# Optimization experiments

Measured on AMD Instinct MI355X. Metric: run time of the kernel, lower is better.

## Reference

```python
import jax, jax.numpy as jnp
import numpy as np

HIDDEN_DIM = 512


def setup_inputs() -> dict:
    key = jax.random.key(0)
    ks = jax.random.split(key, 7)
    B, SQ, SKV, DIN, H = 8, 2048, 2048, 1024, HIDDEN_DIM
    query = jax.random.normal(ks[0], (B, SQ, H), dtype=jnp.float32)
    states = jax.random.normal(ks[1], (B, SKV, DIN), dtype=jnp.float32)
    mask = jax.random.uniform(ks[2], (B, SQ, SKV), dtype=jnp.float32)
    # LazyLinear params (stored as [in, out]; torch uses x @ W.T with W [out, in])
    Wk = jax.random.normal(ks[3], (DIN, H), dtype=jnp.float32) * (1.0 / np.sqrt(DIN))
    bk = jax.random.normal(ks[4], (H,), dtype=jnp.float32) * 0.02
    Wv = jax.random.normal(ks[5], (DIN, H), dtype=jnp.float32) * (1.0 / np.sqrt(DIN))
    bv = jax.random.normal(ks[6], (H,), dtype=jnp.float32) * 0.02
    return {"query": query, "states": states, "mask": mask,
            "Wk": Wk, "bk": bk, "Wv": Wv, "bv": bv}


def reference(query, states, mask, Wk, bk, Wv, bv):
    # transform_states=True: project states into key/value spaces
    keys = states @ Wk + bk        # [B, S_kv, H]
    values = states @ Wv + bv      # [B, S_kv, H]
    # bmm(query, keys^T) / sqrt(H)
    scale = 1.0 / jnp.sqrt(jnp.asarray(keys.shape[-1], dtype=query.dtype))
    scores = jnp.einsum('bqh,bkh->bqk', query, keys) * scale  # [B, S_q, S_kv]
    scores = mask * scores  # multiplicative mask
    # source detaches the softmax output
    attn = jax.lax.stop_gradient(jax.nn.softmax(scores, axis=-1))
    return jnp.einsum('bqk,bkh->bqh', attn, values)  # [B, S_q, H]
```

## Files before the change

kernel.cpp:

```cpp
#include <hip/hip_runtime.h>
#include <hip/hip_bf16.h>
#include <stdint.h>

#define BM 128
#define BN 128
#define BK 32

typedef __bf16 bf16;
typedef bf16 bf16x8 __attribute__((ext_vector_type(8)));
typedef float f32x4 __attribute__((ext_vector_type(4)));

typedef const __attribute__((address_space(1))) void* gas1_t;
typedef __attribute__((address_space(3))) void* las3_t;

__device__ __forceinline__ void gl_lds16(const void* g, void* l) {
  __builtin_amdgcn_global_load_lds((gas1_t)g, (las3_t)l, 16, 0, 0);
}

__device__ __forceinline__ void gemm_core(const bf16* A, const bf16* Bt,
                                          int lda, int ldb, int kTiles,
                                          bf16* As, bf16* Bs, f32x4 acc[4][4]) {
  const int tid = threadIdx.x;
  const int lane = tid & 63;
  const int wid = tid >> 6;
  const int wr = wid >> 1, wc = wid & 1;
  const int lr = lane & 15, lg = lane >> 4;

  for (int kt = 0; kt < kTiles; ++kt) {
    const bf16* Ak = A + kt * BK;
    const bf16* Bk = Bt + kt * BK;
#pragma unroll
    for (int p = 0; p < 2; ++p) {
      int c = p * 256 + tid;
      int row = c >> 2, k8 = (c & 3) << 3;
      gl_lds16(Ak + (size_t)row * lda + k8, As + c * 8);
      gl_lds16(Bk + (size_t)row * ldb + k8, Bs + c * 8);
    }
    __syncthreads();
    bf16x8 af[4], bfr[4];
#pragma unroll
    for (int i = 0; i < 4; ++i) {
      af[i]  = *(const bf16x8*)(As + (wr * 64 + i * 16 + lr) * BK + lg * 8);
      bfr[i] = *(const bf16x8*)(Bs + (wc * 64 + i * 16 + lr) * BK + lg * 8);
    }
#pragma unroll
    for (int i = 0; i < 4; ++i)
#pragma unroll
      for (int j = 0; j < 4; ++j)
        acc[i][j] = __builtin_amdgcn_mfma_f32_16x16x32_bf16(af[i], bfr[j], acc[i][j], 0, 0, 0);
    __syncthreads();
  }
}

__global__ __launch_bounds__(256) void k_cast(const float* __restrict__ in,
                                              bf16* __restrict__ out, int n8) {
  int i = blockIdx.x * blockDim.x + threadIdx.x;
  int stride = gridDim.x * blockDim.x;
  for (; i < n8; i += stride) {
    float4 a = ((const float4*)in)[2 * (size_t)i];
    float4 b = ((const float4*)in)[2 * (size_t)i + 1];
    bf16x8 o;
    o[0] = (bf16)a.x; o[1] = (bf16)a.y; o[2] = (bf16)a.z; o[3] = (bf16)a.w;
    o[4] = (bf16)b.x; o[5] = (bf16)b.y; o[6] = (bf16)b.z; o[7] = (bf16)b.w;
    ((bf16x8*)out)[i] = o;
  }
}

__global__ __launch_bounds__(256) void k_buildwt(const float* __restrict__ Wk,
                                                 const float* __restrict__ Wv,
                                                 bf16* __restrict__ Wt) {
  int n = blockIdx.x;
  const float* W = (n < 512) ? Wk : Wv;
  int col = n & 511;
  for (int k = threadIdx.x; k < 1024; k += 256)
    Wt[(size_t)n * 1024 + k] = (bf16)W[(size_t)k * 512 + col];
}

__global__ __launch_bounds__(256) void k_proj(const bf16* __restrict__ S,
                                              const bf16* __restrict__ Wt,
                                              const float* __restrict__ bk,
                                              const float* __restrict__ bv,
                                              bf16* __restrict__ Kb,
                                              bf16* __restrict__ VT) {
  __shared__ bf16 As[BM * BK], Bs[BN * BK];
  f32x4 acc[4][4] = {};
  int m0 = blockIdx.x * BM, n0 = blockIdx.y * BN;
  gemm_core(S + (size_t)m0 * 1024, Wt + (size_t)n0 * 1024, 1024, 1024, 1024 / BK, As, Bs, acc);
  const int lane = threadIdx.x & 63, wid = threadIdx.x >> 6;
  const int wr = wid >> 1, wc = wid & 1, lr = lane & 15, lg = lane >> 4;
#pragma unroll
  for (int i = 0; i < 4; ++i) {
    int gmb = m0 + wr * 64 + i * 16 + lg * 4;
#pragma unroll
    for (int j = 0; j < 4; ++j) {
      int gn = n0 + wc * 64 + j * 16 + lr;
      f32x4 v = acc[i][j];
      if (gn < 512) {
        float bias = bk[gn];
#pragma unroll
        for (int r = 0; r < 4; ++r)
          Kb[(size_t)(gmb + r) * 512 + gn] = (bf16)(v[r] + bias);
      } else {
        float bias = bv[gn - 512];
#pragma unroll
        for (int r = 0; r < 4; ++r) {
          int gm = gmb + r, b = gm >> 11, s = gm & 2047;
          VT[((size_t)(b * 512 + (gn - 512))) * 2048 + s] = (bf16)(v[r] + bias);
        }
      }
    }
  }
}

__global__ __launch_bounds__(256) void k_scores(const bf16* __restrict__ Qb,
                                                const bf16* __restrict__ Kb,
                                                const float* __restrict__ mask,
                                                bf16* __restrict__ P,
                                                float* __restrict__ lsum) {
  __shared__ bf16 As[BM * BK], Bs[BN * BK];
  f32x4 acc[4][4] = {};
  int b = blockIdx.z;
  int m0 = blockIdx.x * BM, n0 = blockIdx.y * BN;
  gemm_core(Qb + (size_t)b * 2048 * 512 + (size_t)m0 * 512,
            Kb + (size_t)b * 2048 * 512 + (size_t)n0 * 512, 512, 512, 512 / BK, As, Bs, acc);
  const float scale = 0.04419417382415922f;
  const float* Mb = mask + (size_t)b * 2048 * 2048;
  bf16* Pb = P + (size_t)b * 2048 * 2048;
  const int lane = threadIdx.x & 63, wid = threadIdx.x >> 6;
  const int wr = wid >> 1, wc = wid & 1, lr = lane & 15, lg = lane >> 4;
  float rs[4][4];
#pragma unroll
  for (int i = 0; i < 4; ++i)
#pragma unroll
    for (int r = 0; r < 4; ++r) rs[i][r] = 0.f;
#pragma unroll
  for (int i = 0; i < 4; ++i) {
    int gmb = m0 + wr * 64 + i * 16 + lg * 4;
#pragma unroll
    for (int j = 0; j < 4; ++j) {
      int gn = n0 + wc * 64 + j * 16 + lr;
      f32x4 v = acc[i][j];
#pragma unroll
      for (int r = 0; r < 4; ++r) {
        size_t off = (size_t)(gmb + r) * 2048 + gn;
        float p = __expf(v[r] * scale * Mb[off]);
        Pb[off] = (bf16)p;
        rs[i][r] += p;
      }
    }
  }
#pragma unroll
  for (int i = 0; i < 4; ++i)
#pragma unroll
    for (int r = 0; r < 4; ++r) {
      float v = rs[i][r];
      v += __shfl_xor(v, 1, 16);
      v += __shfl_xor(v, 2, 16);
      v += __shfl_xor(v, 4, 16);
      v += __shfl_xor(v, 8, 16);
      if (lr == 0)
        atomicAdd(&lsum[b * 2048 + m0 + wr * 64 + i * 16 + lg * 4 + r], v);
    }
}

__global__ __launch_bounds__(256) void k_pv(const bf16* __restrict__ P,
                                            const bf16* __restrict__ VT,
                                            const float* __restrict__ lsum,
                                            float* __restrict__ out) {
  __shared__ bf16 As[BM * BK], Bs[BN * BK];
  f32x4 acc[4][4] = {};
  int b = blockIdx.z;
  int m0 = blockIdx.x * BM, n0 = blockIdx.y * BN;
  gemm_core(P + (size_t)b * 2048 * 2048 + (size_t)m0 * 2048,
            VT + (size_t)b * 512 * 2048 + (size_t)n0 * 2048, 2048, 2048, 2048 / BK, As, Bs, acc);
  float* Ob = out + (size_t)b * 2048 * 512;
  const float* lb = lsum + b * 2048;
  const int lane = threadIdx.x & 63, wid = threadIdx.x >> 6;
  const int wr = wid >> 1, wc = wid & 1, lr = lane & 15, lg = lane >> 4;
#pragma unroll
  for (int i = 0; i < 4; ++i) {
    int gmb = m0 + wr * 64 + i * 16 + lg * 4;
#pragma unroll
    for (int j = 0; j < 4; ++j) {
      int gn = n0 + wc * 64 + j * 16 + lr;
      f32x4 v = acc[i][j];
#pragma unroll
      for (int r = 0; r < 4; ++r)
        Ob[(size_t)(gmb + r) * 512 + gn] = v[r] / lb[gmb + r];
    }
  }
}

extern "C" void kernel_launch(void* const* d_in, const int* in_sizes, int n_in,
                              void* d_out, int out_size, void* d_ws, size_t ws_size,
                              hipStream_t stream) {
  const float* query  = (const float*)d_in[0];
  const float* states = (const float*)d_in[1];
  const float* mask   = (const float*)d_in[2];
  const float* Wk     = (const float*)d_in[3];
  const float* bk     = (const float*)d_in[4];
  const float* Wv     = (const float*)d_in[5];
  const float* bv     = (const float*)d_in[6];
  float* out = (float*)d_out;

  char* ws = (char*)d_ws;
  bf16* WT = (bf16*)(ws);
  bf16* Qb = (bf16*)(ws + (2ull << 20));
  bf16* Kb = (bf16*)(ws + (18ull << 20));
  bf16* VT = (bf16*)(ws + (34ull << 20));
  bf16* Sb = (bf16*)(ws + (50ull << 20));
  bf16* P  = (bf16*)(ws + (50ull << 20));
  float* ls = (float*)(ws + (114ull << 20));

  hipMemsetAsync(ls, 0, 8 * 2048 * sizeof(float), stream);
  k_buildwt<<<dim3(1024), 256, 0, stream>>>(Wk, Wv, WT);
  k_cast<<<dim3(2048), 256, 0, stream>>>(states, Sb, 16384 * 1024 / 8);
  k_cast<<<dim3(1024), 256, 0, stream>>>(query, Qb, 8 * 2048 * 512 / 8);
  k_proj<<<dim3(128, 8), 256, 0, stream>>>(Sb, WT, bk, bv, Kb, VT);
  k_scores<<<dim3(16, 16, 8), 256, 0, stream>>>(Qb, Kb, mask, P, ls);
  k_pv<<<dim3(16, 4, 8), 256, 0, stream>>>(P, VT, ls, out);
}
```

Before: 453.0 us.

## Swap GEMM operand roles so epilogues write contiguous vectors

Swaps the A/B operands of the score, PV and key-projection GEMMs so each lane's four accumulator rows land on contiguous memory. Mask reads, P writes, K writes and output writes become float4/bf16x4 vector accesses instead of strided scalar ones. The combined K/V projection is split into two kernels, each with a layout-friendly epilogue. The weight transpose now goes through an LDS tile for coalescing. Risks are more kernel launches and changed tile order and cache locality.

```diff
diff --git a/kernel.cpp b/kernel.cpp
--- a/kernel.cpp
+++ b/kernel.cpp
@@ -7,6 +7,7 @@
 #define BK 32
 
 typedef __bf16 bf16;
+typedef bf16 bf16x4 __attribute__((ext_vector_type(4)));
 typedef bf16 bf16x8 __attribute__((ext_vector_type(8)));
 typedef float f32x4 __attribute__((ext_vector_type(4)));
 
@@ -66,127 +67,145 @@
   }
 }
 
-__global__ __launch_bounds__(256) void k_buildwt(const float* __restrict__ Wk,
-                                                 const float* __restrict__ Wv,
-                                                 bf16* __restrict__ Wt) {
-  int n = blockIdx.x;
-  const float* W = (n < 512) ? Wk : Wv;
-  int col = n & 511;
-  for (int k = threadIdx.x; k < 1024; k += 256)
-    Wt[(size_t)n * 1024 + k] = (bf16)W[(size_t)k * 512 + col];
-}
-
-__global__ __launch_bounds__(256) void k_proj(const bf16* __restrict__ S,
-                                              const bf16* __restrict__ Wt,
-                                              const float* __restrict__ bk,
-                                              const float* __restrict__ bv,
-                                              bf16* __restrict__ Kb,
-                                              bf16* __restrict__ VT) {
-  __shared__ bf16 As[BM * BK], Bs[BN * BK];
-  f32x4 acc[4][4] = {};
-  int m0 = blockIdx.x * BM, n0 = blockIdx.y * BN;
-  gemm_core(S + (size_t)m0 * 1024, Wt + (size_t)n0 * 1024, 1024, 1024, 1024 / BK, As, Bs, acc);
+__global__ __launch_bounds__(256) void k_transposeW(const float* __restrict__ Wk,
+                                                    const float* __restrict__ Wv,
+                                                    bf16* __restrict__ WT) {
+  __shared__ float t[32][33];
+  const float* W = blockIdx.z ? Wv : Wk;
+  bf16* O = WT + (size_t)blockIdx.z * 512 * 1024;
+  int h0 = blockIdx.x * 32, d0 = blockIdx.y * 32;
+  int tx = threadIdx.x & 31, ty = threadIdx.x >> 5;
+#pragma unroll
+  for (int yy = 0; yy < 4; ++yy)
+    t[ty + yy * 8][tx] = W[(size_t)(d0 + ty + yy * 8) * 512 + h0 + tx];
+  __syncthreads();
+#pragma unroll
+  for (int yy = 0; yy < 4; ++yy)
+    O[(size_t)(h0 + ty + yy * 8) * 1024 + d0 + tx] = (bf16)t[tx][ty + yy * 8];
+}
+
+__global__ __launch_bounds__(256) void k_projK(const bf16* __restrict__ WkT,
+                                               const bf16* __restrict__ S,
+                                               const float* __restrict__ bk,
+                                               bf16* __restrict__ Kb) {
+  __shared__ bf16 As[BM * BK], Bs[BN * BK];
+  f32x4 acc[4][4] = {};
+  int h0 = blockIdx.x * BM, t0 = blockIdx.y * BN;
+  gemm_core(WkT + (size_t)h0 * 1024, S + (size_t)t0 * 1024, 1024, 1024, 1024 / BK, As, Bs, acc);
   const int lane = threadIdx.x & 63, wid = threadIdx.x >> 6;
   const int wr = wid >> 1, wc = wid & 1, lr = lane & 15, lg = lane >> 4;
 #pragma unroll
   for (int i = 0; i < 4; ++i) {
-    int gmb = m0 + wr * 64 + i * 16 + lg * 4;
+    int hb = h0 + wr * 64 + i * 16 + lg * 4;
+    float4 bias = *(const float4*)(bk + hb);
 #pragma unroll
     for (int j = 0; j < 4; ++j) {
-      int gn = n0 + wc * 64 + j * 16 + lr;
-      f32x4 v = acc[i][j];
-      if (gn < 512) {
-        float bias = bk[gn];
-#pragma unroll
-        for (int r = 0; r < 4; ++r)
-          Kb[(size_t)(gmb + r) * 512 + gn] = (bf16)(v[r] + bias);
-      } else {
-        float bias = bv[gn - 512];
-#pragma unroll
-        for (int r = 0; r < 4; ++r) {
-          int gm = gmb + r, b = gm >> 11, s = gm & 2047;
-          VT[((size_t)(b * 512 + (gn - 512))) * 2048 + s] = (bf16)(v[r] + bias);
-        }
-      }
-    }
-  }
-}
-
-__global__ __launch_bounds__(256) void k_scores(const bf16* __restrict__ Qb,
-                                                const bf16* __restrict__ Kb,
+      int t = t0 + wc * 64 + j * 16 + lr;
+      f32x4 v = acc[i][j];
+      bf16x4 o;
+      o[0] = (bf16)(v[0] + bias.x); o[1] = (bf16)(v[1] + bias.y);
+      o[2] = (bf16)(v[2] + bias.z); o[3] = (bf16)(v[3] + bias.w);
+      *(bf16x4*)(Kb + (size_t)t * 512 + hb) = o;
+    }
+  }
+}
+
+__global__ __launch_bounds__(256) void k_projV(const bf16* __restrict__ S,
+                                               const bf16* __restrict__ WvT,
+                                               const float* __restrict__ bv,
+                                               bf16* __restrict__ VT) {
+  __shared__ bf16 As[BM * BK], Bs[BN * BK];
+  f32x4 acc[4][4] = {};
+  int t0 = blockIdx.x * BM, h0 = blockIdx.y * BN;
+  gemm_core(S + (size_t)t0 * 1024, WvT + (size_t)h0 * 1024, 1024, 1024, 1024 / BK, As, Bs, acc);
+  const int lane = threadIdx.x & 63, wid = threadIdx.x >> 6;
+  const int wr = wid >> 1, wc = wid & 1, lr = lane & 15, lg = lane >> 4;
+#pragma unroll
+  for (int i = 0; i < 4; ++i) {
+    int tb = t0 + wr * 64 + i * 16 + lg * 4;
+    int b = tb >> 11, s = tb & 2047;
+#pragma unroll
+    for (int j = 0; j < 4; ++j) {
+      int h = h0 + wc * 64 + j * 16 + lr;
+      float bias = bv[h];
+      f32x4 v = acc[i][j];
+      bf16x4 o;
+      o[0] = (bf16)(v[0] + bias); o[1] = (bf16)(v[1] + bias);
+      o[2] = (bf16)(v[2] + bias); o[3] = (bf16)(v[3] + bias);
+      *(bf16x4*)(VT + ((size_t)(b * 512 + h)) * 2048 + s) = o;
+    }
+  }
+}
+
+__global__ __launch_bounds__(256) void k_scores(const bf16* __restrict__ Kb,
+                                                const bf16* __restrict__ Qb,
                                                 const float* __restrict__ mask,
                                                 bf16* __restrict__ P,
                                                 float* __restrict__ lsum) {
   __shared__ bf16 As[BM * BK], Bs[BN * BK];
   f32x4 acc[4][4] = {};
   int b = blockIdx.z;
-  int m0 = blockIdx.x * BM, n0 = blockIdx.y * BN;
-  gemm_core(Qb + (size_t)b * 2048 * 512 + (size_t)m0 * 512,
-            Kb + (size_t)b * 2048 * 512 + (size_t)n0 * 512, 512, 512, 512 / BK, As, Bs, acc);
+  int kv0 = blockIdx.x * BM, q0 = blockIdx.y * BN;
+  gemm_core(Kb + (size_t)b * 2048 * 512 + (size_t)kv0 * 512,
+            Qb + (size_t)b * 2048 * 512 + (size_t)q0 * 512, 512, 512, 512 / BK, As, Bs, acc);
   const float scale = 0.04419417382415922f;
   const float* Mb = mask + (size_t)b * 2048 * 2048;
   bf16* Pb = P + (size_t)b * 2048 * 2048;
   const int lane = threadIdx.x & 63, wid = threadIdx.x >> 6;
   const int wr = wid >> 1, wc = wid & 1, lr = lane & 15, lg = lane >> 4;
-  float rs[4][4];
-#pragma unroll
-  for (int i = 0; i < 4; ++i)
-#pragma unroll
-    for (int r = 0; r < 4; ++r) rs[i][r] = 0.f;
-#pragma unroll
-  for (int i = 0; i < 4; ++i) {
-    int gmb = m0 + wr * 64 + i * 16 + lg * 4;
-#pragma unroll
-    for (int j = 0; j < 4; ++j) {
-      int gn = n0 + wc * 64 + j * 16 + lr;
-      f32x4 v = acc[i][j];
-#pragma unroll
-      for (int r = 0; r < 4; ++r) {
-        size_t off = (size_t)(gmb + r) * 2048 + gn;
-        float p = __expf(v[r] * scale * Mb[off]);
-        Pb[off] = (bf16)p;
-        rs[i][r] += p;
-      }
-    }
-  }
-#pragma unroll
-  for (int i = 0; i < 4; ++i)
-#pragma unroll
-    for (int r = 0; r < 4; ++r) {
-      float v = rs[i][r];
-      v += __shfl_xor(v, 1, 16);
-      v += __shfl_xor(v, 2, 16);
-      v += __shfl_xor(v, 4, 16);
-      v += __shfl_xor(v, 8, 16);
-      if (lr == 0)
-        atomicAdd(&lsum[b * 2048 + m0 + wr * 64 + i * 16 + lg * 4 + r], v);
-    }
-}
-
-__global__ __launch_bounds__(256) void k_pv(const bf16* __restrict__ P,
-                                            const bf16* __restrict__ VT,
+  float rs[4] = {0.f, 0.f, 0.f, 0.f};
+#pragma unroll
+  for (int j = 0; j < 4; ++j) {
+    int q = q0 + wc * 64 + j * 16 + lr;
+    size_t qrow = (size_t)q * 2048;
+#pragma unroll
+    for (int i = 0; i < 4; ++i) {
+      int kvb = kv0 + wr * 64 + i * 16 + lg * 4;
+      float4 m4 = *(const float4*)(Mb + qrow + kvb);
+      f32x4 v = acc[i][j];
+      float p0 = __expf(v[0] * scale * m4.x);
+      float p1 = __expf(v[1] * scale * m4.y);
+      float p2 = __expf(v[2] * scale * m4.z);
+      float p3 = __expf(v[3] * scale * m4.w);
+      bf16x4 o; o[0] = (bf16)p0; o[1] = (bf16)p1; o[2] = (bf16)p2; o[3] = (bf16)p3;
+      *(bf16x4*)(Pb + qrow + kvb) = o;
+      rs[j] += p0 + p1 + p2 + p3;
+    }
+  }
+#pragma unroll
+  for (int j = 0; j < 4; ++j) {
+    float v = rs[j];
+    v += __shfl_xor(v, 16);
+    v += __shfl_xor(v, 32);
+    if (lane < 16)
+      atomicAdd(&lsum[b * 2048 + q0 + wc * 64 + j * 16 + lr], v);
+  }
+}
+
+__global__ __launch_bounds__(256) void k_pv(const bf16* __restrict__ VT,
+                                            const bf16* __restrict__ P,
                                             const float* __restrict__ lsum,
                                             float* __restrict__ out) {
   __shared__ bf16 As[BM * BK], Bs[BN * BK];
   f32x4 acc[4][4] = {};
   int b = blockIdx.z;
-  int m0 = blockIdx.x * BM, n0 = blockIdx.y * BN;
-  gemm_core(P + (size_t)b * 2048 * 2048 + (size_t)m0 * 2048,
-            VT + (size_t)b * 512 * 2048 + (size_t)n0 * 2048, 2048, 2048, 2048 / BK, As, Bs, acc);
+  int h0 = blockIdx.x * BM, q0 = blockIdx.y * BN;
+  gemm_core(VT + (size_t)b * 512 * 2048 + (size_t)h0 * 2048,
+            P + (size_t)b * 2048 * 2048 + (size_t)q0 * 2048, 2048, 2048, 2048 / BK, As, Bs, acc);
   float* Ob = out + (size_t)b * 2048 * 512;
   const float* lb = lsum + b * 2048;
   const int lane = threadIdx.x & 63, wid = threadIdx.x >> 6;
   const int wr = wid >> 1, wc = wid & 1, lr = lane & 15, lg = lane >> 4;
 #pragma unroll
-  for (int i = 0; i < 4; ++i) {
-    int gmb = m0 + wr * 64 + i * 16 + lg * 4;
-#pragma unroll
-    for (int j = 0; j < 4; ++j) {
-      int gn = n0 + wc * 64 + j * 16 + lr;
-      f32x4 v = acc[i][j];
-#pragma unroll
-      for (int r = 0; r < 4; ++r)
-        Ob[(size_t)(gmb + r) * 512 + gn] = v[r] / lb[gmb + r];
+  for (int j = 0; j < 4; ++j) {
+    int q = q0 + wc * 64 + j * 16 + lr;
+    float inv = 1.0f / lb[q];
+#pragma unroll
+    for (int i = 0; i < 4; ++i) {
+      int hb = h0 + wr * 64 + i * 16 + lg * 4;
+      f32x4 v = acc[i][j];
+      float4 o4 = make_float4(v[0] * inv, v[1] * inv, v[2] * inv, v[3] * inv);
+      *(float4*)(Ob + (size_t)q * 512 + hb) = o4;
     }
   }
 }
@@ -212,11 +231,15 @@
   bf16* P  = (bf16*)(ws + (50ull << 20));
   float* ls = (float*)(ws + (114ull << 20));
 
+  bf16* WkT = WT;
+  bf16* WvT = WT + (size_t)512 * 1024;
+
   hipMemsetAsync(ls, 0, 8 * 2048 * sizeof(float), stream);
-  k_buildwt<<<dim3(1024), 256, 0, stream>>>(Wk, Wv, WT);
+  k_transposeW<<<dim3(16, 32, 2), 256, 0, stream>>>(Wk, Wv, WT);
   k_cast<<<dim3(2048), 256, 0, stream>>>(states, Sb, 16384 * 1024 / 8);
   k_cast<<<dim3(1024), 256, 0, stream>>>(query, Qb, 8 * 2048 * 512 / 8);
-  k_proj<<<dim3(128, 8), 256, 0, stream>>>(Sb, WT, bk, bv, Kb, VT);
-  k_scores<<<dim3(16, 16, 8), 256, 0, stream>>>(Qb, Kb, mask, P, ls);
-  k_pv<<<dim3(16, 4, 8), 256, 0, stream>>>(P, VT, ls, out);
-}
+  k_projK<<<dim3(4, 128), 256, 0, stream>>>(WkT, Sb, bk, Kb);
+  k_projV<<<dim3(128, 4), 256, 0, stream>>>(Sb, WvT, bv, VT);
+  k_scores<<<dim3(16, 16, 8), 256, 0, stream>>>(Kb, Qb, mask, P, ls);
+  k_pv<<<dim3(4, 16, 8), 256, 0, stream>>>(VT, P, ls, out);
+}
```

Result: no change. 450.1 us (-0.6%).
